# Kernel optimization log

Measured on AMD Instinct MI355X. Metric: run time of the kernel, lower is better.

Reference implementation:

```python
import jax, jax.numpy as jnp
import numpy as np

OFFSET_BINS = np.array([0.0, 0.00794435329, 0.0158887021, 0.0238330509, 0.0317773996,
                        0.0397217484, 0.0476660972, 0.0556104459, 0.0635547947,
                        0.0714991435, 0.08], dtype=np.float32)
BIN_WEIGHTS = jnp.array([0.16652107, 0.21488856, 0.37031708, 0.55618503, 0.75124664,
                         0.93943357, 1.07824539, 1.19423112, 1.55731375, 2.34173634],
                        dtype=jnp.float32)
RADIUS = 0.005
FAR = 1.0e5
EPS = 1e-7


def setup_inputs():
    key = jax.random.key(0)
    ks = jax.random.split(key, 10)
    B, N, M, C = 4, 2048, 4096, 5
    return {
        'pred_grasps': jax.random.normal(ks[0], (B, N, 4, 4), jnp.float32) * 0.1,
        'pred_scores': jax.random.uniform(ks[1], (B, N, 1), jnp.float32, 1e-4, 1.0 - 1e-4),
        'pred_points': jax.random.uniform(ks[2], (B, N, 3), jnp.float32) * 0.1,
        'grasp_width_head': jax.random.normal(ks[3], (B, 10, N), jnp.float32),
        'pos_contact_points': jax.random.uniform(ks[4], (B, M, 3), jnp.float32) * 0.1,
        'pos_contact_width': jax.random.uniform(ks[5], (B, M), jnp.float32) * 0.08,
        'pos_contact_rot': jax.random.normal(ks[6], (B, M, 3, 3), jnp.float32),
        'pos_contact_trans': jax.random.uniform(ks[7], (B, M, 3), jnp.float32) * 0.1,
        'gripper_control_points': jax.random.normal(ks[8], (1, C, 3), jnp.float32) * 0.05,
        'gripper_control_points_sym': jax.random.normal(ks[9], (1, C, 3), jnp.float32) * 0.05,
        'epoch': 0,
    }


def _gather(a, idx):
    # a: (B, M, ...), idx: (B, N) -> (B, N, ...)
    return jax.vmap(lambda x, j: x[j])(a, idx)


def _pairwise_sq(a, b):
    # a: (B,N,3), b: (B,M,3) -> (B,N,M) squared distances via norm expansion
    an = jnp.sum(a * a, -1)
    bn = jnp.sum(b * b, -1)
    cross = jnp.einsum('bnd,bmd->bnm', a, b)
    return jnp.maximum(an[:, :, None] + bn[:, None, :] - 2.0 * cross, 0.0)


def _pair_min_cp(P, G):
    # P,G: (B,N,C,3) control point sets -> (B,N) min_j sum_{c,d}(P_i - G_j)^2
    pn = jnp.sum(P * P, axis=(2, 3))
    gn = jnp.sum(G * G, axis=(2, 3))
    cross = jnp.einsum('bicd,bjcd->bij', P, G)  # (B,N,N)
    sq = pn[:, :, None] + gn[:, None, :] - 2.0 * cross
    return jnp.min(sq, axis=2)


def _forward(pred_grasps, pred_scores, pred_points, grasp_width_head,
             pos_contact_points, pos_contact_width, pos_contact_rot,
             pos_contact_trans, gripper_control_points, gripper_control_points_sym):
    B, N, _ = pred_points.shape
    # ---- labels: nearest GT contact per predicted point (nsample=1) ----
    d2 = _pairwise_sq(pred_points, pos_contact_points)          # (B,N,M)
    idx = jnp.argmin(d2, axis=2)                                 # (B,N)
    min_d2 = jnp.take_along_axis(d2, idx[:, :, None], axis=2)[..., 0]
    width_label = _gather(pos_contact_width, idx)[..., None]     # (B,N,1)
    success = (min_d2 < RADIUS ** 2).astype(jnp.float32)[..., None]  # (B,N,1)
    rot_label = _gather(pos_contact_rot, idx)                    # (B,N,3,3)
    trans_label = _gather(pos_contact_trans, idx)                # (B,N,3)

    pos_in_view = jnp.clip(jnp.sum(success, axis=1), 1.0, None)  # (B,1)

    # ---- binary score loss with balanced pos/neg sampling ----
    p = jnp.clip(pred_scores, EPS, 1.0 - EPS)
    bce = -(success * jnp.log(p) + (1.0 - success) * jnp.log(1.0 - p))[..., 0]  # (B,N)
    pos = success[..., 0]
    neg = 1.0 - pos
    n_pos = jnp.sum(pos, axis=1)                                 # (B,)
    r = jax.random.uniform(jax.random.key(42), (B, N))
    pri = jnp.where(neg > 0.5, r, jnp.inf)
    rank = jnp.argsort(jnp.argsort(pri, axis=1), axis=1)         # random ranks over negatives
    k = jnp.where(n_pos > 0, n_pos, 2.0)
    sel_neg = ((rank < k[:, None]) & (neg > 0.5)).astype(jnp.float32)
    sel = pos + sel_neg
    bin_ce_loss = jnp.mean(jnp.sum(bce * sel, axis=1) / jnp.maximum(jnp.sum(sel, axis=1), 1.0))

    # ---- width loss: multihot bins + weighted BCE-with-logits ----
    lo = jnp.asarray(OFFSET_BINS[:-1])
    hi = jnp.asarray(OFFSET_BINS[1:])
    multihot = ((width_label >= lo) & (width_label < hi)).astype(jnp.float32)  # (B,N,10)
    x = jnp.transpose(grasp_width_head, (0, 2, 1))               # (B,N,10)
    bcew = jnp.maximum(x, 0.0) - x * multihot + jnp.log1p(jnp.exp(-jnp.abs(x)))
    wl = jnp.mean(BIN_WEIGHTS[None, None, :] * bcew, axis=2)     # (B,N)
    width_loss = jnp.mean(jnp.sum(wl * pos, axis=1, keepdims=True) / pos_in_view)

    # ---- ADD-S loss ----
    mask = success > 0.5                                          # (B,N,1)
    rot_l = jnp.where(mask[..., None], rot_label, FAR)
    trans_l = jnp.where(mask, trans_label, FAR)
    cp = gripper_control_points[0]                                # (C,3)
    cps = gripper_control_points_sym[0]
    pred_rot = pred_grasps[:, :, :3, :3]
    pred_trans = pred_grasps[:, :, :3, 3]
    P = jnp.einsum('bnij,cj->bnci', pred_rot, cp) + pred_trans[:, :, None, :]
    G = jnp.einsum('bnij,cj->bnci', rot_l, cp) + trans_l[:, :, None, :]
    Gs = jnp.einsum('bnij,cj->bnci', rot_l, cps) + trans_l[:, :, None, :]
    m = jnp.minimum(_pair_min_cp(P, G), _pair_min_cp(P, Gs))     # (B,N)
    min_adds = pos * jnp.sqrt(jnp.maximum(m, 0.0) + 1e-12)
    adds = jnp.sum(pred_scores[..., 0] * min_adds, axis=1) / pos_in_view[:, 0]
    adds_loss = jnp.mean(adds)

    total_loss = bin_ce_loss + width_loss + 3.0 * adds_loss
    return total_loss, bin_ce_loss, width_loss, adds_loss


def reference(pred_grasps, pred_scores, pred_points, grasp_width_head,
              pos_contact_points, pos_contact_width, pos_contact_rot,
              pos_contact_trans, gripper_control_points, gripper_control_points_sym, epoch):
    return _forward(pred_grasps, pred_scores, pred_points, grasp_width_head,
                    pos_contact_points, pos_contact_width, pos_contact_rot,
                    pos_contact_trans, gripper_control_points, gripper_control_points_sym)
```

## Files before the change

### kernel.cpp

```cpp
#include <hip/hip_runtime.h>
#include <math.h>

#define B_ 4
#define N_ 2048
#define M_ 4096

__constant__ float c_LO[10] = {0.0f, 0.00794435329f, 0.0158887021f, 0.0238330509f,
                               0.0317773996f, 0.0397217484f, 0.0476660972f,
                               0.0556104459f, 0.0635547947f, 0.0714991435f};
__constant__ float c_HI[10] = {0.00794435329f, 0.0158887021f, 0.0238330509f,
                               0.0317773996f, 0.0397217484f, 0.0476660972f,
                               0.0556104459f, 0.0635547947f, 0.0714991435f, 0.08f};
__constant__ float c_BW[10] = {0.16652107f, 0.21488856f, 0.37031708f, 0.55618503f,
                               0.75124664f, 0.93943357f, 1.07824539f, 1.19423112f,
                               1.55731375f, 2.34173634f};

#define R2_ 2.5e-05f
#define FAR_ 100000.0f
#define EPS_ 1e-07f

__device__ inline unsigned rotl32(unsigned x, int d) { return (x << d) | (x >> (32 - d)); }

__device__ inline void threefry2x32_42(unsigned x0, unsigned x1, unsigned& o0, unsigned& o1) {
    const unsigned k0 = 0u, k1 = 42u;
    const unsigned k2 = k0 ^ k1 ^ 0x1BD11BDAu;
    const unsigned ks[3] = {k0, k1, k2};
    const int rot[2][4] = {{13, 15, 26, 6}, {17, 29, 16, 24}};
    unsigned v0 = x0 + k0;
    unsigned v1 = x1 + k1;
#pragma unroll
    for (int i = 0; i < 5; ++i) {
        const int* r = rot[i & 1];
#pragma unroll
        for (int j = 0; j < 4; ++j) {
            v0 += v1;
            v1 = rotl32(v1, r[j]);
            v1 ^= v0;
        }
        v0 += ks[(i + 1) % 3];
        v1 += ks[(i + 2) % 3] + (unsigned)(i + 1);
    }
    o0 = v0; o1 = v1;
}

__device__ inline float bits_to_uniform(unsigned bits) {
    float f = __uint_as_float((bits >> 9) | 0x3f800000u) - 1.0f;
    return fmaxf(0.0f, f);
}

__device__ inline float jax_uniform_r(int flat) {
    unsigned o0, o1;
    if (flat < 4096) {
        threefry2x32_42((unsigned)flat, (unsigned)(flat + 4096), o0, o1);
        return bits_to_uniform(o0);
    } else {
        threefry2x32_42((unsigned)(flat - 4096), (unsigned)flat, o0, o1);
        return bits_to_uniform(o1);
    }
}

__global__ __launch_bounds__(256, 4) void nn_prep_kernel(
        const float* __restrict__ ppts, const float* __restrict__ pcp,
        const float* __restrict__ pred_grasps,
        const float* __restrict__ rot, const float* __restrict__ trans,
        const float* __restrict__ cp, const float* __restrict__ cps,
        int* __restrict__ idx_out, float* __restrict__ d2_out,
        float* __restrict__ Pout, float* __restrict__ Gout) {
    int blk = blockIdx.x;
    int b = blk / (N_ / 8);
    int tile = blk % (N_ / 8);
    int tid = threadIdx.x;
    int ig = tid & 1;
    int part = tid >> 1;
    int i0 = tile * 8 + ig * 4;

    float ax[4], ay[4], az[4], an[4];
#pragma unroll
    for (int ii = 0; ii < 4; ++ii) {
        const float* pp = ppts + ((size_t)b * N_ + i0 + ii) * 3;
        ax[ii] = pp[0]; ay[ii] = pp[1]; az[ii] = pp[2];
        an[ii] = ax[ii] * ax[ii] + ay[ii] * ay[ii] + az[ii] * az[ii];
    }

    const float4* pb4 = reinterpret_cast<const float4*>(pcp + (size_t)b * M_ * 3);
    float best[4] = {INFINITY, INFINITY, INFINITY, INFINITY};
    int bidx[4] = {0, 0, 0, 0};
    for (int g = 0; g < 8; ++g) {
        int grp = g * 128 + part;
        float4 q0 = pb4[grp * 3 + 0];
        float4 q1 = pb4[grp * 3 + 1];
        float4 q2 = pb4[grp * 3 + 2];
        float px[4] = {q0.x, q0.w, q1.z, q2.y};
        float py[4] = {q0.y, q1.x, q1.w, q2.z};
        float pz[4] = {q0.z, q1.y, q2.x, q2.w};
#pragma unroll
        for (int k = 0; k < 4; ++k) {
            float bn = px[k] * px[k] + py[k] * py[k] + pz[k] * pz[k];
            int j = grp * 4 + k;
#pragma unroll
            for (int ii = 0; ii < 4; ++ii) {
                float cross = ax[ii] * px[k] + ay[ii] * py[k] + az[ii] * pz[k];
                float d = an[ii] + bn - 2.0f * cross;
                d = fmaxf(d, 0.0f);
                if (d < best[ii]) { best[ii] = d; bidx[ii] = j; }
            }
        }
    }

    __shared__ float sd[8][128];
    __shared__ int si[8][128];
#pragma unroll
    for (int ii = 0; ii < 4; ++ii) {
        sd[ig * 4 + ii][part] = best[ii];
        si[ig * 4 + ii][part] = bidx[ii];
    }
    __syncthreads();

    if (tid < 8) {
        int n = tile * 8 + tid;
        float bb = INFINITY;
        int bi = 0x7fffffff;
        for (int p = 0; p < 128; ++p) {
            float dv = sd[tid][p];
            int iv = si[tid][p];
            if (dv < bb || (dv == bb && iv < bi)) { bb = dv; bi = iv; }
        }
        idx_out[b * N_ + n] = bi;
        d2_out[b * N_ + n] = bb;

        size_t i = (size_t)b * N_ + n;
        const float* g = pred_grasps + i * 16;
        float R[3][3] = {{g[0], g[1], g[2]}, {g[4], g[5], g[6]}, {g[8], g[9], g[10]}};
        float t[3] = {g[3], g[7], g[11]};

        float* P = Pout + i * 16;
        float pn = 0.0f;
#pragma unroll
        for (int c = 0; c < 5; ++c) {
            float cx = cp[c * 3], cy = cp[c * 3 + 1], cz = cp[c * 3 + 2];
#pragma unroll
            for (int kk = 0; kk < 3; ++kk) {
                float v = R[kk][0] * cx + R[kk][1] * cy + R[kk][2] * cz + t[kk];
                P[c * 3 + kk] = v;
                pn += v * v;
            }
        }
        P[15] = pn;

        bool succ = bb < R2_;
        float RL[3][3], TL[3];
        if (succ) {
            const float* rl = rot + ((size_t)b * M_ + bi) * 9;
#pragma unroll
            for (int a = 0; a < 3; ++a)
#pragma unroll
                for (int c2 = 0; c2 < 3; ++c2) RL[a][c2] = rl[a * 3 + c2];
            const float* tl = trans + ((size_t)b * M_ + bi) * 3;
            TL[0] = tl[0]; TL[1] = tl[1]; TL[2] = tl[2];
        } else {
#pragma unroll
            for (int a = 0; a < 3; ++a) {
#pragma unroll
                for (int c2 = 0; c2 < 3; ++c2) RL[a][c2] = FAR_;
                TL[a] = FAR_;
            }
        }

        float* G = Gout + i * 32;
        float gn = 0.0f, gsn = 0.0f;
#pragma unroll
        for (int c = 0; c < 5; ++c) {
            float cx = cp[c * 3], cy = cp[c * 3 + 1], cz = cp[c * 3 + 2];
#pragma unroll
            for (int kk = 0; kk < 3; ++kk) {
                float v = RL[kk][0] * cx + RL[kk][1] * cy + RL[kk][2] * cz + TL[kk];
                G[c * 3 + kk] = v;
                gn += v * v;
            }
        }
        G[15] = gn;
#pragma unroll
        for (int c = 0; c < 5; ++c) {
            float cx = cps[c * 3], cy = cps[c * 3 + 1], cz = cps[c * 3 + 2];
#pragma unroll
            for (int kk = 0; kk < 3; ++kk) {
                float v = RL[kk][0] * cx + RL[kk][1] * cy + RL[kk][2] * cz + TL[kk];
                G[16 + c * 3 + kk] = v;
                gsn += v * v;
            }
        }
        G[31] = gsn;
    }
}

__global__ __launch_bounds__(256) void rank_kernel(const float* __restrict__ d2w,
                                                   float* __restrict__ selws,
                                                   int* __restrict__ done_cnt) {
    if (blockIdx.x == 0 && threadIdx.x == 0) *done_cnt = 0;
    int blk = blockIdx.x;
    int b = blk / (N_ / 16);
    int tile = blk % (N_ / 16);
    int tid = threadIdx.x;
    int n_local = tid & 15;
    int part = tid >> 4;

    __shared__ __align__(16) float pri[N_];
    __shared__ int cnt_sh[16][17];
    __shared__ int s_npos;
    if (tid == 0) s_npos = 0;
    __syncthreads();

    int lp = 0;
    for (int q = tid; q < N_; q += 256) {
        bool pos = d2w[b * N_ + q] < R2_;
        pri[q] = pos ? INFINITY : jax_uniform_r(b * N_ + q);
        if (pos) lp++;
    }
    atomicAdd(&s_npos, lp);
    __syncthreads();

    int n = tile * 16 + n_local;
    float ra = pri[n];

    int cnt = 0;
    const float4* p4 = reinterpret_cast<const float4*>(pri);
    for (int o = 0; o < 8; ++o) {
        float4 v[4];
#pragma unroll
        for (int k = 0; k < 4; ++k) v[k] = p4[part + (o * 4 + k) * 16];
#pragma unroll
        for (int k = 0; k < 4; ++k) {
            int qb = (part + (o * 4 + k) * 16) * 4;
            cnt += ((v[k].x < ra) || (v[k].x == ra && (qb + 0) < n)) ? 1 : 0;
            cnt += ((v[k].y < ra) || (v[k].y == ra && (qb + 1) < n)) ? 1 : 0;
            cnt += ((v[k].z < ra) || (v[k].z == ra && (qb + 2) < n)) ? 1 : 0;
            cnt += ((v[k].w < ra) || (v[k].w == ra && (qb + 3) < n)) ? 1 : 0;
        }
    }
    cnt_sh[part][n_local] = cnt;
    __syncthreads();

    if (tid < 16) {
        int tot = 0;
#pragma unroll
        for (int p = 0; p < 16; ++p) tot += cnt_sh[p][tid];
        int npos = s_npos;
        int kk = (npos > 0) ? npos : 2;
        int n2 = tile * 16 + tid;
        float r2 = pri[n2];
        selws[b * N_ + n2] = (r2 == INFINITY) ? 1.0f : ((tot < kk) ? 1.0f : 0.0f);
    }
}

__global__ __launch_bounds__(256, 4) void adds_kernel(const float* __restrict__ Parr,
                                                      const float* __restrict__ Garr,
                                                      float* __restrict__ mOut) {
    int blk = blockIdx.x;
    int b = blk / (N_ / 8);
    int tile = blk % (N_ / 8);
    int ig = threadIdx.x & 1;
    int part = threadIdx.x >> 1;
    int i0 = tile * 8 + ig * 4;

    const float4* P4 = reinterpret_cast<const float4*>(Parr) + ((size_t)b * N_ + i0) * 4;
    float Pv[4][16];
#pragma unroll
    for (int ii = 0; ii < 4; ++ii) {
#pragma unroll
        for (int q = 0; q < 4; ++q) {
            float4 t4 = P4[ii * 4 + q];
            Pv[ii][q * 4 + 0] = t4.x; Pv[ii][q * 4 + 1] = t4.y;
            Pv[ii][q * 4 + 2] = t4.z; Pv[ii][q * 4 + 3] = t4.w;
        }
    }

    const float4* Gb4 = reinterpret_cast<const float4*>(Garr) + (size_t)b * N_ * 8;
    float best[4] = {INFINITY, INFINITY, INFINITY, INFINITY};
    int j0 = part * 16;
    for (int j = j0; j < j0 + 16; ++j) {
        const float4* G4 = Gb4 + (size_t)j * 8;
        float gg[16];
#pragma unroll
        for (int q = 0; q < 4; ++q) {
            float4 t4 = G4[q];
            gg[q * 4 + 0] = t4.x; gg[q * 4 + 1] = t4.y;
            gg[q * 4 + 2] = t4.z; gg[q * 4 + 3] = t4.w;
        }
        {
            float d[4] = {0.0f, 0.0f, 0.0f, 0.0f};
#pragma unroll
            for (int q = 0; q < 15; ++q)
#pragma unroll
                for (int ii = 0; ii < 4; ++ii) d[ii] += Pv[ii][q] * gg[q];
#pragma unroll
            for (int ii = 0; ii < 4; ++ii) {
                float s = Pv[ii][15] + gg[15] - 2.0f * d[ii];
                best[ii] = fminf(best[ii], s);
            }
        }
#pragma unroll
        for (int q = 0; q < 4; ++q) {
            float4 t4 = G4[4 + q];
            gg[q * 4 + 0] = t4.x; gg[q * 4 + 1] = t4.y;
            gg[q * 4 + 2] = t4.z; gg[q * 4 + 3] = t4.w;
        }
        {
            float d[4] = {0.0f, 0.0f, 0.0f, 0.0f};
#pragma unroll
            for (int q = 0; q < 15; ++q)
#pragma unroll
                for (int ii = 0; ii < 4; ++ii) d[ii] += Pv[ii][q] * gg[q];
#pragma unroll
            for (int ii = 0; ii < 4; ++ii) {
                float s = Pv[ii][15] + gg[15] - 2.0f * d[ii];
                best[ii] = fminf(best[ii], s);
            }
        }
    }
    __shared__ float sm[128][9];
#pragma unroll
    for (int ii = 0; ii < 4; ++ii) sm[part][ig * 4 + ii] = best[ii];
    __syncthreads();
    if (threadIdx.x < 8) {
        float bb = sm[0][threadIdx.x];
#pragma unroll
        for (int q = 1; q < 128; ++q) bb = fminf(bb, sm[q][threadIdx.x]);
        mOut[b * N_ + tile * 8 + threadIdx.x] = bb;
    }
}

__global__ __launch_bounds__(256) void finalize_kernel(
        const float* __restrict__ scores, const float* __restrict__ gwh,
        const float* __restrict__ pcw, const int* __restrict__ idxw,
        const float* __restrict__ d2w, const float* __restrict__ mw,
        const float* __restrict__ selws,
        float* __restrict__ partials, int* __restrict__ done_cnt,
        float* __restrict__ out) {
    int blk = blockIdx.x;
    int b = blk >> 3;
    int part = blk & 7;
    int tid = threadIdx.x;
    int n = part * 256 + tid;
    __shared__ float wsum[4][5];

    float sc = scores[b * N_ + n];
    float pcl = fminf(fmaxf(sc, EPS_), 0.9999999f);
    bool pos = d2w[b * N_ + n] < R2_;
    float s = pos ? 1.0f : 0.0f;
    float bce = -(s * logf(pcl) + (1.0f - s) * logf(1.0f - pcl));
    float selv = selws[b * N_ + n];
    float sum_sel = selv;
    float sum_bce = bce * selv;
    float sum_pos = s;
    float sum_wl = 0.0f, sum_adds = 0.0f;
    if (pos) {
        int jx = idxw[b * N_ + n];
        float w = pcw[b * M_ + jx];
        float acc = 0.0f;
#pragma unroll
        for (int jb = 0; jb < 10; ++jb) {
            float x = gwh[((size_t)b * 10 + jb) * N_ + n];
            float mh = (w >= c_LO[jb] && w < c_HI[jb]) ? 1.0f : 0.0f;
            float bw = fmaxf(x, 0.0f) - x * mh + log1pf(expf(-fabsf(x)));
            acc += c_BW[jb] * bw;
        }
        sum_wl = acc * 0.1f;
        float mv = mw[b * N_ + n];
        sum_adds = sc * sqrtf(fmaxf(mv, 0.0f) + 1e-12f);
    }

    float v0 = sum_sel, v1 = sum_bce, v2 = sum_wl, v3 = sum_adds, v4 = sum_pos;
#pragma unroll
    for (int off = 32; off > 0; off >>= 1) {
        v0 += __shfl_down(v0, off);
        v1 += __shfl_down(v1, off);
        v2 += __shfl_down(v2, off);
        v3 += __shfl_down(v3, off);
        v4 += __shfl_down(v4, off);
    }
    int wv = tid >> 6, lane = tid & 63;
    if (lane == 0) {
        wsum[wv][0] = v0; wsum[wv][1] = v1; wsum[wv][2] = v2; wsum[wv][3] = v3; wsum[wv][4] = v4;
    }
    __syncthreads();
    if (tid == 0) {
        float t0 = 0, t1 = 0, t2 = 0, t3 = 0, t4 = 0;
#pragma unroll
        for (int w = 0; w < 4; ++w) {
            t0 += wsum[w][0]; t1 += wsum[w][1]; t2 += wsum[w][2]; t3 += wsum[w][3]; t4 += wsum[w][4];
        }
        float* pp = partials + (size_t)blk * 5;
        pp[0] = t0; pp[1] = t1; pp[2] = t2; pp[3] = t3; pp[4] = t4;
        __threadfence();
        int old = atomicAdd(done_cnt, 1);
        if (old == B_ * 8 - 1) {
            __threadfence();
            float bin = 0, wid = 0, ad = 0;
#pragma unroll
            for (int b2 = 0; b2 < B_; ++b2) {
                float u0 = 0, u1 = 0, u2 = 0, u3 = 0, u4 = 0;
#pragma unroll
                for (int p2 = 0; p2 < 8; ++p2) {
                    const float* q = partials + (size_t)(b2 * 8 + p2) * 5;
                    u0 += q[0]; u1 += q[1]; u2 += q[2]; u3 += q[3]; u4 += q[4];
                }
                float piv = fmaxf(u4, 1.0f);
                bin += u1 / fmaxf(u0, 1.0f);
                wid += u2 / piv;
                ad  += u3 / piv;
            }
            bin *= 0.25f; wid *= 0.25f; ad *= 0.25f;
            out[0] = bin + wid + 3.0f * ad;
            out[1] = bin;
            out[2] = wid;
            out[3] = ad;
        }
    }
}

extern "C" void kernel_launch(void* const* d_in, const int* in_sizes, int n_in,
                              void* d_out, int out_size, void* d_ws, size_t ws_size,
                              hipStream_t stream) {
    const float* pred_grasps = (const float*)d_in[0];
    const float* pred_scores = (const float*)d_in[1];
    const float* pred_points = (const float*)d_in[2];
    const float* gwh         = (const float*)d_in[3];
    const float* pcp         = (const float*)d_in[4];
    const float* pcw         = (const float*)d_in[5];
    const float* pcr         = (const float*)d_in[6];
    const float* pct         = (const float*)d_in[7];
    const float* cp          = (const float*)d_in[8];
    const float* cps         = (const float*)d_in[9];
    (void)in_sizes; (void)n_in; (void)out_size; (void)ws_size;

    float* ws = (float*)d_ws;
    int*   idxw  = (int*)ws;
    float* d2w   = ws + 8192;
    float* Pw    = ws + 16384;
    float* Gw    = Pw + 131072;
    float* mw    = Gw + 262144;
    float* selws = mw + 8192;
    float* parts = selws + 8192;
    int*   done  = (int*)(parts + 160);
    float* outp  = (float*)d_out;

    hipLaunchKernelGGL(nn_prep_kernel, dim3(B_ * (N_ / 8)), dim3(256), 0, stream,
                       pred_points, pcp, pred_grasps, pcr, pct, cp, cps,
                       idxw, d2w, Pw, Gw);
    hipLaunchKernelGGL(rank_kernel, dim3(B_ * (N_ / 16)), dim3(256), 0, stream,
                       d2w, selws, done);
    hipLaunchKernelGGL(adds_kernel, dim3(B_ * (N_ / 8)), dim3(256), 0, stream,
                       Pw, Gw, mw);
    hipLaunchKernelGGL(finalize_kernel, dim3(B_ * 8), dim3(256), 0, stream,
                       pred_scores, gwh, pcw, idxw, d2w, mw, selws, parts, done, outp);
}
```

Baseline: 162.8 us.

## Fuse rank, adds and finalize kernels into one launch with counter-gated finalize

Merges the rank, ADD-S min-distance and finalize kernels into one mega kernel that dispatches on block index. Finalize blocks spin on a global counter until all producer blocks finish. The ADD-S part now stages G tiles in shared memory and gives each thread 2 P rows instead of 4, so all threads reuse the staged G. This removes two kernel launches and lets the rank and adds work run concurrently, at the cost of a spin-wait that depends on the finalize blocks being dispatched last and extra syncthreads per tile.

```diff
diff --git a/kernel.cpp b/kernel.cpp
--- a/kernel.cpp
+++ b/kernel.cpp
@@ -4,6 +4,11 @@
 #define B_ 4
 #define N_ 2048
 #define M_ 4096
+
+#define ADDS_BLOCKS (B_ * (N_ / 8))
+#define RANK_BLOCKS (B_ * (N_ / 16))
+#define FIN_BLOCKS (B_ * 8)
+#define PROD_BLOCKS (ADDS_BLOCKS + RANK_BLOCKS)
 
 __constant__ float c_LO[10] = {0.0f, 0.00794435329f, 0.0158887021f, 0.0238330509f,
                                0.0317773996f, 0.0397217484f, 0.0476660972f,
@@ -65,7 +70,9 @@
         const float* __restrict__ rot, const float* __restrict__ trans,
         const float* __restrict__ cp, const float* __restrict__ cps,
         int* __restrict__ idx_out, float* __restrict__ d2_out,
-        float* __restrict__ Pout, float* __restrict__ Gout) {
+        float* __restrict__ Pout, float* __restrict__ Gout,
+        int* __restrict__ counters) {
+    if (blockIdx.x == 0 && threadIdx.x == 0) { counters[0] = 0; counters[1] = 0; }
     int blk = blockIdx.x;
     int b = blk / (N_ / 8);
     int tile = blk % (N_ / 8);
@@ -193,227 +200,257 @@
     }
 }
 
-__global__ __launch_bounds__(256) void rank_kernel(const float* __restrict__ d2w,
-                                                   float* __restrict__ selws,
-                                                   int* __restrict__ done_cnt) {
-    if (blockIdx.x == 0 && threadIdx.x == 0) *done_cnt = 0;
-    int blk = blockIdx.x;
-    int b = blk / (N_ / 16);
-    int tile = blk % (N_ / 16);
-    int tid = threadIdx.x;
-    int n_local = tid & 15;
-    int part = tid >> 4;
-
-    __shared__ __align__(16) float pri[N_];
-    __shared__ int cnt_sh[16][17];
-    __shared__ int s_npos;
-    if (tid == 0) s_npos = 0;
-    __syncthreads();
-
-    int lp = 0;
-    for (int q = tid; q < N_; q += 256) {
-        bool pos = d2w[b * N_ + q] < R2_;
-        pri[q] = pos ? INFINITY : jax_uniform_r(b * N_ + q);
-        if (pos) lp++;
-    }
-    atomicAdd(&s_npos, lp);
-    __syncthreads();
-
-    int n = tile * 16 + n_local;
-    float ra = pri[n];
-
-    int cnt = 0;
-    const float4* p4 = reinterpret_cast<const float4*>(pri);
-    for (int o = 0; o < 8; ++o) {
-        float4 v[4];
-#pragma unroll
-        for (int k = 0; k < 4; ++k) v[k] = p4[part + (o * 4 + k) * 16];
-#pragma unroll
-        for (int k = 0; k < 4; ++k) {
-            int qb = (part + (o * 4 + k) * 16) * 4;
-            cnt += ((v[k].x < ra) || (v[k].x == ra && (qb + 0) < n)) ? 1 : 0;
-            cnt += ((v[k].y < ra) || (v[k].y == ra && (qb + 1) < n)) ? 1 : 0;
-            cnt += ((v[k].z < ra) || (v[k].z == ra && (qb + 2) < n)) ? 1 : 0;
-            cnt += ((v[k].w < ra) || (v[k].w == ra && (qb + 3) < n)) ? 1 : 0;
-        }
-    }
-    cnt_sh[part][n_local] = cnt;
-    __syncthreads();
-
-    if (tid < 16) {
-        int tot = 0;
-#pragma unroll
-        for (int p = 0; p < 16; ++p) tot += cnt_sh[p][tid];
-        int npos = s_npos;
-        int kk = (npos > 0) ? npos : 2;
-        int n2 = tile * 16 + tid;
-        float r2 = pri[n2];
-        selws[b * N_ + n2] = (r2 == INFINITY) ? 1.0f : ((tot < kk) ? 1.0f : 0.0f);
-    }
-}
-
-__global__ __launch_bounds__(256, 4) void adds_kernel(const float* __restrict__ Parr,
-                                                      const float* __restrict__ Garr,
-                                                      float* __restrict__ mOut) {
-    int blk = blockIdx.x;
-    int b = blk / (N_ / 8);
-    int tile = blk % (N_ / 8);
-    int ig = threadIdx.x & 1;
-    int part = threadIdx.x >> 1;
-    int i0 = tile * 8 + ig * 4;
-
-    const float4* P4 = reinterpret_cast<const float4*>(Parr) + ((size_t)b * N_ + i0) * 4;
-    float Pv[4][16];
-#pragma unroll
-    for (int ii = 0; ii < 4; ++ii) {
-#pragma unroll
-        for (int q = 0; q < 4; ++q) {
-            float4 t4 = P4[ii * 4 + q];
-            Pv[ii][q * 4 + 0] = t4.x; Pv[ii][q * 4 + 1] = t4.y;
-            Pv[ii][q * 4 + 2] = t4.z; Pv[ii][q * 4 + 3] = t4.w;
-        }
-    }
-
-    const float4* Gb4 = reinterpret_cast<const float4*>(Garr) + (size_t)b * N_ * 8;
-    float best[4] = {INFINITY, INFINITY, INFINITY, INFINITY};
-    int j0 = part * 16;
-    for (int j = j0; j < j0 + 16; ++j) {
-        const float4* G4 = Gb4 + (size_t)j * 8;
-        float gg[16];
-#pragma unroll
-        for (int q = 0; q < 4; ++q) {
-            float4 t4 = G4[q];
-            gg[q * 4 + 0] = t4.x; gg[q * 4 + 1] = t4.y;
-            gg[q * 4 + 2] = t4.z; gg[q * 4 + 3] = t4.w;
-        }
-        {
-            float d[4] = {0.0f, 0.0f, 0.0f, 0.0f};
-#pragma unroll
-            for (int q = 0; q < 15; ++q)
-#pragma unroll
-                for (int ii = 0; ii < 4; ++ii) d[ii] += Pv[ii][q] * gg[q];
-#pragma unroll
-            for (int ii = 0; ii < 4; ++ii) {
-                float s = Pv[ii][15] + gg[15] - 2.0f * d[ii];
-                best[ii] = fminf(best[ii], s);
-            }
-        }
-#pragma unroll
-        for (int q = 0; q < 4; ++q) {
-            float4 t4 = G4[4 + q];
-            gg[q * 4 + 0] = t4.x; gg[q * 4 + 1] = t4.y;
-            gg[q * 4 + 2] = t4.z; gg[q * 4 + 3] = t4.w;
-        }
-        {
-            float d[4] = {0.0f, 0.0f, 0.0f, 0.0f};
-#pragma unroll
-            for (int q = 0; q < 15; ++q)
-#pragma unroll
-                for (int ii = 0; ii < 4; ++ii) d[ii] += Pv[ii][q] * gg[q];
-#pragma unroll
-            for (int ii = 0; ii < 4; ++ii) {
-                float s = Pv[ii][15] + gg[15] - 2.0f * d[ii];
-                best[ii] = fminf(best[ii], s);
-            }
-        }
-    }
-    __shared__ float sm[128][9];
-#pragma unroll
-    for (int ii = 0; ii < 4; ++ii) sm[part][ig * 4 + ii] = best[ii];
-    __syncthreads();
-    if (threadIdx.x < 8) {
-        float bb = sm[0][threadIdx.x];
-#pragma unroll
-        for (int q = 1; q < 128; ++q) bb = fminf(bb, sm[q][threadIdx.x]);
-        mOut[b * N_ + tile * 8 + threadIdx.x] = bb;
-    }
-}
-
-__global__ __launch_bounds__(256) void finalize_kernel(
+__global__ __launch_bounds__(256, 4) void mega_kernel(
+        const float* __restrict__ Parr, const float* __restrict__ Garr,
+        float* __restrict__ mOut,
+        const float* __restrict__ d2w, float* __restrict__ selws,
         const float* __restrict__ scores, const float* __restrict__ gwh,
         const float* __restrict__ pcw, const int* __restrict__ idxw,
-        const float* __restrict__ d2w, const float* __restrict__ mw,
-        const float* __restrict__ selws,
-        float* __restrict__ partials, int* __restrict__ done_cnt,
+        float* __restrict__ partials, int* __restrict__ counters,
         float* __restrict__ out) {
-    int blk = blockIdx.x;
-    int b = blk >> 3;
-    int part = blk & 7;
+    __shared__ __align__(16) char smem[18464];
+    int bid = blockIdx.x;
     int tid = threadIdx.x;
-    int n = part * 256 + tid;
-    __shared__ float wsum[4][5];
-
-    float sc = scores[b * N_ + n];
-    float pcl = fminf(fmaxf(sc, EPS_), 0.9999999f);
-    bool pos = d2w[b * N_ + n] < R2_;
-    float s = pos ? 1.0f : 0.0f;
-    float bce = -(s * logf(pcl) + (1.0f - s) * logf(1.0f - pcl));
-    float selv = selws[b * N_ + n];
-    float sum_sel = selv;
-    float sum_bce = bce * selv;
-    float sum_pos = s;
-    float sum_wl = 0.0f, sum_adds = 0.0f;
-    if (pos) {
-        int jx = idxw[b * N_ + n];
-        float w = pcw[b * M_ + jx];
-        float acc = 0.0f;
-#pragma unroll
-        for (int jb = 0; jb < 10; ++jb) {
-            float x = gwh[((size_t)b * 10 + jb) * N_ + n];
-            float mh = (w >= c_LO[jb] && w < c_HI[jb]) ? 1.0f : 0.0f;
-            float bw = fmaxf(x, 0.0f) - x * mh + log1pf(expf(-fabsf(x)));
-            acc += c_BW[jb] * bw;
-        }
-        sum_wl = acc * 0.1f;
-        float mv = mw[b * N_ + n];
-        sum_adds = sc * sqrtf(fmaxf(mv, 0.0f) + 1e-12f);
-    }
-
-    float v0 = sum_sel, v1 = sum_bce, v2 = sum_wl, v3 = sum_adds, v4 = sum_pos;
-#pragma unroll
-    for (int off = 32; off > 0; off >>= 1) {
-        v0 += __shfl_down(v0, off);
-        v1 += __shfl_down(v1, off);
-        v2 += __shfl_down(v2, off);
-        v3 += __shfl_down(v3, off);
-        v4 += __shfl_down(v4, off);
-    }
-    int wv = tid >> 6, lane = tid & 63;
-    if (lane == 0) {
-        wsum[wv][0] = v0; wsum[wv][1] = v1; wsum[wv][2] = v2; wsum[wv][3] = v3; wsum[wv][4] = v4;
-    }
-    __syncthreads();
-    if (tid == 0) {
-        float t0 = 0, t1 = 0, t2 = 0, t3 = 0, t4 = 0;
-#pragma unroll
-        for (int w = 0; w < 4; ++w) {
-            t0 += wsum[w][0]; t1 += wsum[w][1]; t2 += wsum[w][2]; t3 += wsum[w][3]; t4 += wsum[w][4];
-        }
-        float* pp = partials + (size_t)blk * 5;
-        pp[0] = t0; pp[1] = t1; pp[2] = t2; pp[3] = t3; pp[4] = t4;
+
+    if (bid < ADDS_BLOCKS) {
+        int b = bid >> 8;
+        int tile_i = bid & 255;
+        int i0 = tile_i * 8;
+        int ip = tid & 3;
+        int jp = tid >> 2;
+
+        const float4* P4 = reinterpret_cast<const float4*>(Parr) +
+                           ((size_t)b * N_ + i0 + ip * 2) * 4;
+        float Pv[2][16];
+#pragma unroll
+        for (int h = 0; h < 2; ++h)
+#pragma unroll
+            for (int q = 0; q < 4; ++q) {
+                float4 v = P4[h * 4 + q];
+                Pv[h][q * 4 + 0] = v.x; Pv[h][q * 4 + 1] = v.y;
+                Pv[h][q * 4 + 2] = v.z; Pv[h][q * 4 + 3] = v.w;
+            }
+
+        float* sG = (float*)smem;
+        const float4* Gb4 = reinterpret_cast<const float4*>(Garr) + (size_t)b * N_ * 8;
+        float best[2] = {INFINITY, INFINITY};
+
+        for (int jt = 0; jt < 16; ++jt) {
+            __syncthreads();
+            const float4* src = Gb4 + (size_t)jt * 1024;
+#pragma unroll
+            for (int t = 0; t < 4; ++t) {
+                int idx = t * 256 + tid;
+                int r = idx >> 3, q = idx & 7;
+                float4 v = src[idx];
+                *reinterpret_cast<float4*>(&sG[r * 36 + q * 4]) = v;
+            }
+            __syncthreads();
+#pragma unroll
+            for (int jj = 0; jj < 2; ++jj) {
+                const float* row = &sG[(jj * 64 + jp) * 36];
+                float gg[16];
+#pragma unroll
+                for (int q = 0; q < 4; ++q) {
+                    float4 v = *reinterpret_cast<const float4*>(&row[q * 4]);
+                    gg[q * 4 + 0] = v.x; gg[q * 4 + 1] = v.y;
+                    gg[q * 4 + 2] = v.z; gg[q * 4 + 3] = v.w;
+                }
+                {
+                    float d0 = 0.0f, d1 = 0.0f;
+#pragma unroll
+                    for (int q = 0; q < 15; ++q) {
+                        d0 += Pv[0][q] * gg[q];
+                        d1 += Pv[1][q] * gg[q];
+                    }
+                    best[0] = fminf(best[0], Pv[0][15] + gg[15] - 2.0f * d0);
+                    best[1] = fminf(best[1], Pv[1][15] + gg[15] - 2.0f * d1);
+                }
+#pragma unroll
+                for (int q = 0; q < 4; ++q) {
+                    float4 v = *reinterpret_cast<const float4*>(&row[16 + q * 4]);
+                    gg[q * 4 + 0] = v.x; gg[q * 4 + 1] = v.y;
+                    gg[q * 4 + 2] = v.z; gg[q * 4 + 3] = v.w;
+                }
+                {
+                    float d0 = 0.0f, d1 = 0.0f;
+#pragma unroll
+                    for (int q = 0; q < 15; ++q) {
+                        d0 += Pv[0][q] * gg[q];
+                        d1 += Pv[1][q] * gg[q];
+                    }
+                    best[0] = fminf(best[0], Pv[0][15] + gg[15] - 2.0f * d0);
+                    best[1] = fminf(best[1], Pv[1][15] + gg[15] - 2.0f * d1);
+                }
+            }
+        }
+
+        __syncthreads();
+        float* sm = (float*)smem;
+        sm[jp * 9 + ip * 2 + 0] = best[0];
+        sm[jp * 9 + ip * 2 + 1] = best[1];
+        __syncthreads();
+        if (tid < 8) {
+            float bb = sm[tid];
+            for (int q = 1; q < 64; ++q) bb = fminf(bb, sm[q * 9 + tid]);
+            mOut[b * N_ + i0 + tid] = bb;
+        }
+        __syncthreads();
+        if (tid == 0) {
+            __threadfence();
+            __hip_atomic_fetch_add(&counters[0], 1, __ATOMIC_RELEASE,
+                                   __HIP_MEMORY_SCOPE_AGENT);
+        }
+    } else if (bid < PROD_BLOCKS) {
+        int rid = bid - ADDS_BLOCKS;
+        int b = rid / (N_ / 16);
+        int tile = rid % (N_ / 16);
+        int n_local = tid & 15;
+        int part = tid >> 4;
+
+        float* pri = (float*)smem;
+        int* cnt_sh = (int*)(smem + 8192);
+        __shared__ int s_npos;
+        if (tid == 0) s_npos = 0;
+        __syncthreads();
+
+        int lp = 0;
+        for (int q = tid; q < N_; q += 256) {
+            bool pos = d2w[b * N_ + q] < R2_;
+            pri[q] = pos ? INFINITY : jax_uniform_r(b * N_ + q);
+            if (pos) lp++;
+        }
+        atomicAdd(&s_npos, lp);
+        __syncthreads();
+
+        int n = tile * 16 + n_local;
+        float ra = pri[n];
+
+        int cnt = 0;
+        const float4* p4 = reinterpret_cast<const float4*>(pri);
+        for (int o = 0; o < 8; ++o) {
+            float4 v[4];
+#pragma unroll
+            for (int k = 0; k < 4; ++k) v[k] = p4[part + (o * 4 + k) * 16];
+#pragma unroll
+            for (int k = 0; k < 4; ++k) {
+                int qb = (part + (o * 4 + k) * 16) * 4;
+                cnt += ((v[k].x < ra) || (v[k].x == ra && (qb + 0) < n)) ? 1 : 0;
+                cnt += ((v[k].y < ra) || (v[k].y == ra && (qb + 1) < n)) ? 1 : 0;
+                cnt += ((v[k].z < ra) || (v[k].z == ra && (qb + 2) < n)) ? 1 : 0;
+                cnt += ((v[k].w < ra) || (v[k].w == ra && (qb + 3) < n)) ? 1 : 0;
+            }
+        }
+        cnt_sh[part * 17 + n_local] = cnt;
+        __syncthreads();
+
+        if (tid < 16) {
+            int tot = 0;
+#pragma unroll
+            for (int p = 0; p < 16; ++p) tot += cnt_sh[p * 17 + tid];
+            int npos = s_npos;
+            int kk = (npos > 0) ? npos : 2;
+            int n2 = tile * 16 + tid;
+            float r2 = pri[n2];
+            selws[b * N_ + n2] = (r2 == INFINITY) ? 1.0f : ((tot < kk) ? 1.0f : 0.0f);
+        }
+        __syncthreads();
+        if (tid == 0) {
+            __threadfence();
+            __hip_atomic_fetch_add(&counters[0], 1, __ATOMIC_RELEASE,
+                                   __HIP_MEMORY_SCOPE_AGENT);
+        }
+    } else {
+        int fid = bid - PROD_BLOCKS;
+        int b = fid >> 3;
+        int part = fid & 7;
+        int n = part * 256 + tid;
+        __shared__ float wsum[4][5];
+
+        if (tid == 0) {
+            while (__hip_atomic_load(&counters[0], __ATOMIC_ACQUIRE,
+                                     __HIP_MEMORY_SCOPE_AGENT) < PROD_BLOCKS) {
+                __builtin_amdgcn_s_sleep(2);
+            }
+        }
+        __syncthreads();
         __threadfence();
-        int old = atomicAdd(done_cnt, 1);
-        if (old == B_ * 8 - 1) {
+
+        float sc = scores[b * N_ + n];
+        float pcl = fminf(fmaxf(sc, EPS_), 0.9999999f);
+        bool pos = d2w[b * N_ + n] < R2_;
+        float s = pos ? 1.0f : 0.0f;
+        float bce = -(s * logf(pcl) + (1.0f - s) * logf(1.0f - pcl));
+        float selv = selws[b * N_ + n];
+        float sum_sel = selv;
+        float sum_bce = bce * selv;
+        float sum_pos = s;
+        float sum_wl = 0.0f, sum_adds = 0.0f;
+        if (pos) {
+            int jx = idxw[b * N_ + n];
+            float w = pcw[b * M_ + jx];
+            float acc = 0.0f;
+#pragma unroll
+            for (int jb = 0; jb < 10; ++jb) {
+                float x = gwh[((size_t)b * 10 + jb) * N_ + n];
+                float mh = (w >= c_LO[jb] && w < c_HI[jb]) ? 1.0f : 0.0f;
+                float bw = fmaxf(x, 0.0f) - x * mh + log1pf(expf(-fabsf(x)));
+                acc += c_BW[jb] * bw;
+            }
+            sum_wl = acc * 0.1f;
+            float mv = mOut[b * N_ + n];
+            sum_adds = sc * sqrtf(fmaxf(mv, 0.0f) + 1e-12f);
+        }
+
+        float v0 = sum_sel, v1 = sum_bce, v2 = sum_wl, v3 = sum_adds, v4 = sum_pos;
+#pragma unroll
+        for (int off = 32; off > 0; off >>= 1) {
+            v0 += __shfl_down(v0, off);
+            v1 += __shfl_down(v1, off);
+            v2 += __shfl_down(v2, off);
+            v3 += __shfl_down(v3, off);
+            v4 += __shfl_down(v4, off);
+        }
+        int wv = tid >> 6, lane = tid & 63;
+        if (lane == 0) {
+            wsum[wv][0] = v0; wsum[wv][1] = v1; wsum[wv][2] = v2;
+            wsum[wv][3] = v3; wsum[wv][4] = v4;
+        }
+        __syncthreads();
+        if (tid == 0) {
+            float t0 = 0, t1 = 0, t2 = 0, t3 = 0, t4 = 0;
+#pragma unroll
+            for (int w = 0; w < 4; ++w) {
+                t0 += wsum[w][0]; t1 += wsum[w][1]; t2 += wsum[w][2];
+                t3 += wsum[w][3]; t4 += wsum[w][4];
+            }
+            float* pp = partials + (size_t)fid * 5;
+            pp[0] = t0; pp[1] = t1; pp[2] = t2; pp[3] = t3; pp[4] = t4;
             __threadfence();
-            float bin = 0, wid = 0, ad = 0;
-#pragma unroll
-            for (int b2 = 0; b2 < B_; ++b2) {
-                float u0 = 0, u1 = 0, u2 = 0, u3 = 0, u4 = 0;
-#pragma unroll
-                for (int p2 = 0; p2 < 8; ++p2) {
-                    const float* q = partials + (size_t)(b2 * 8 + p2) * 5;
-                    u0 += q[0]; u1 += q[1]; u2 += q[2]; u3 += q[3]; u4 += q[4];
+            int old = __hip_atomic_fetch_add(&counters[1], 1, __ATOMIC_ACQ_REL,
+                                             __HIP_MEMORY_SCOPE_AGENT);
+            if (old == FIN_BLOCKS - 1) {
+                __threadfence();
+                float bin = 0, wid = 0, ad = 0;
+#pragma unroll
+                for (int b2 = 0; b2 < B_; ++b2) {
+                    float u0 = 0, u1 = 0, u2 = 0, u3 = 0, u4 = 0;
+#pragma unroll
+                    for (int p2 = 0; p2 < 8; ++p2) {
+                        const float* q = partials + (size_t)(b2 * 8 + p2) * 5;
+                        u0 += q[0]; u1 += q[1]; u2 += q[2]; u3 += q[3]; u4 += q[4];
+                    }
+                    float piv = fmaxf(u4, 1.0f);
+                    bin += u1 / fmaxf(u0, 1.0f);
+                    wid += u2 / piv;
+                    ad  += u3 / piv;
                 }
-                float piv = fmaxf(u4, 1.0f);
-                bin += u1 / fmaxf(u0, 1.0f);
-                wid += u2 / piv;
-                ad  += u3 / piv;
-            }
-            bin *= 0.25f; wid *= 0.25f; ad *= 0.25f;
-            out[0] = bin + wid + 3.0f * ad;
-            out[1] = bin;
-            out[2] = wid;
-            out[3] = ad;
+                bin *= 0.25f; wid *= 0.25f; ad *= 0.25f;
+                out[0] = bin + wid + 3.0f * ad;
+                out[1] = bin;
+                out[2] = wid;
+                out[3] = ad;
+            }
         }
     }
 }
@@ -441,16 +478,13 @@
     float* mw    = Gw + 262144;
     float* selws = mw + 8192;
     float* parts = selws + 8192;
-    int*   done  = (int*)(parts + 160);
+    int*   ctrs  = (int*)(parts + 160);
     float* outp  = (float*)d_out;
 
     hipLaunchKernelGGL(nn_prep_kernel, dim3(B_ * (N_ / 8)), dim3(256), 0, stream,
                        pred_points, pcp, pred_grasps, pcr, pct, cp, cps,
-                       idxw, d2w, Pw, Gw);
-    hipLaunchKernelGGL(rank_kernel, dim3(B_ * (N_ / 16)), dim3(256), 0, stream,
-                       d2w, selws, done);
-    hipLaunchKernelGGL(adds_kernel, dim3(B_ * (N_ / 8)), dim3(256), 0, stream,
-                       Pw, Gw, mw);
-    hipLaunchKernelGGL(finalize_kernel, dim3(B_ * 8), dim3(256), 0, stream,
-                       pred_scores, gwh, pcw, idxw, d2w, mw, selws, parts, done, outp);
-}
+                       idxw, d2w, Pw, Gw, ctrs);
+    hipLaunchKernelGGL(mega_kernel, dim3(PROD_BLOCKS + FIN_BLOCKS), dim3(256), 0, stream,
+                       Pw, Gw, mw, d2w, selws,
+                       pred_scores, gwh, pcw, idxw, parts, ctrs, outp);
+}
```

New measurement: 187.8 us. +15.4%, slower.

## Transpose G layout for coalesced adds loads and fold rank into finalize

Applied to the files above, without the earlier changes.

G control-point sets are now stored component-major (32 x N per batch), so the adds kernel can give each lane its own j and read coalesced loads. Each wave handles 2 predictions and reduces with wave shuffles instead of a shared-memory min. The separate rank kernel is removed and its selection counting moves into finalize, which saves one launch. The cost is that each finalize thread now does a serial 2048-element comparison loop across only 32 blocks, which may become the critical path.

```diff
diff --git a/kernel.cpp b/kernel.cpp
--- a/kernel.cpp
+++ b/kernel.cpp
@@ -65,7 +65,9 @@
         const float* __restrict__ rot, const float* __restrict__ trans,
         const float* __restrict__ cp, const float* __restrict__ cps,
         int* __restrict__ idx_out, float* __restrict__ d2_out,
-        float* __restrict__ Pout, float* __restrict__ Gout) {
+        float* __restrict__ Pout, float* __restrict__ Gt,
+        int* __restrict__ counters) {
+    if (blockIdx.x == 0 && threadIdx.x == 0) { counters[0] = 0; counters[1] = 0; }
     int blk = blockIdx.x;
     int b = blk / (N_ / 8);
     int tile = blk % (N_ / 8);
@@ -166,7 +168,7 @@
             }
         }
 
-        float* G = Gout + i * 32;
+        float* gtb = Gt + (size_t)b * 32 * N_ + n;
         float gn = 0.0f, gsn = 0.0f;
 #pragma unroll
         for (int c = 0; c < 5; ++c) {
@@ -174,158 +176,76 @@
 #pragma unroll
             for (int kk = 0; kk < 3; ++kk) {
                 float v = RL[kk][0] * cx + RL[kk][1] * cy + RL[kk][2] * cz + TL[kk];
-                G[c * 3 + kk] = v;
+                gtb[(size_t)(c * 3 + kk) * N_] = v;
                 gn += v * v;
             }
         }
-        G[15] = gn;
+        gtb[(size_t)15 * N_] = gn;
 #pragma unroll
         for (int c = 0; c < 5; ++c) {
             float cx = cps[c * 3], cy = cps[c * 3 + 1], cz = cps[c * 3 + 2];
 #pragma unroll
             for (int kk = 0; kk < 3; ++kk) {
                 float v = RL[kk][0] * cx + RL[kk][1] * cy + RL[kk][2] * cz + TL[kk];
-                G[16 + c * 3 + kk] = v;
+                gtb[(size_t)(16 + c * 3 + kk) * N_] = v;
                 gsn += v * v;
             }
         }
-        G[31] = gsn;
-    }
-}
-
-__global__ __launch_bounds__(256) void rank_kernel(const float* __restrict__ d2w,
-                                                   float* __restrict__ selws,
-                                                   int* __restrict__ done_cnt) {
-    if (blockIdx.x == 0 && threadIdx.x == 0) *done_cnt = 0;
-    int blk = blockIdx.x;
-    int b = blk / (N_ / 16);
-    int tile = blk % (N_ / 16);
-    int tid = threadIdx.x;
-    int n_local = tid & 15;
-    int part = tid >> 4;
-
-    __shared__ __align__(16) float pri[N_];
-    __shared__ int cnt_sh[16][17];
-    __shared__ int s_npos;
-    if (tid == 0) s_npos = 0;
-    __syncthreads();
-
-    int lp = 0;
-    for (int q = tid; q < N_; q += 256) {
-        bool pos = d2w[b * N_ + q] < R2_;
-        pri[q] = pos ? INFINITY : jax_uniform_r(b * N_ + q);
-        if (pos) lp++;
-    }
-    atomicAdd(&s_npos, lp);
-    __syncthreads();
-
-    int n = tile * 16 + n_local;
-    float ra = pri[n];
-
-    int cnt = 0;
-    const float4* p4 = reinterpret_cast<const float4*>(pri);
-    for (int o = 0; o < 8; ++o) {
-        float4 v[4];
-#pragma unroll
-        for (int k = 0; k < 4; ++k) v[k] = p4[part + (o * 4 + k) * 16];
-#pragma unroll
-        for (int k = 0; k < 4; ++k) {
-            int qb = (part + (o * 4 + k) * 16) * 4;
-            cnt += ((v[k].x < ra) || (v[k].x == ra && (qb + 0) < n)) ? 1 : 0;
-            cnt += ((v[k].y < ra) || (v[k].y == ra && (qb + 1) < n)) ? 1 : 0;
-            cnt += ((v[k].z < ra) || (v[k].z == ra && (qb + 2) < n)) ? 1 : 0;
-            cnt += ((v[k].w < ra) || (v[k].w == ra && (qb + 3) < n)) ? 1 : 0;
-        }
-    }
-    cnt_sh[part][n_local] = cnt;
-    __syncthreads();
-
-    if (tid < 16) {
-        int tot = 0;
-#pragma unroll
-        for (int p = 0; p < 16; ++p) tot += cnt_sh[p][tid];
-        int npos = s_npos;
-        int kk = (npos > 0) ? npos : 2;
-        int n2 = tile * 16 + tid;
-        float r2 = pri[n2];
-        selws[b * N_ + n2] = (r2 == INFINITY) ? 1.0f : ((tot < kk) ? 1.0f : 0.0f);
+        gtb[(size_t)31 * N_] = gsn;
     }
 }
 
 __global__ __launch_bounds__(256, 4) void adds_kernel(const float* __restrict__ Parr,
-                                                      const float* __restrict__ Garr,
+                                                      const float* __restrict__ Gt,
                                                       float* __restrict__ mOut) {
     int blk = blockIdx.x;
     int b = blk / (N_ / 8);
     int tile = blk % (N_ / 8);
-    int ig = threadIdx.x & 1;
-    int part = threadIdx.x >> 1;
-    int i0 = tile * 8 + ig * 4;
+    int w = threadIdx.x >> 6;
+    int lane = threadIdx.x & 63;
+    int i0 = tile * 8 + w * 2;
 
     const float4* P4 = reinterpret_cast<const float4*>(Parr) + ((size_t)b * N_ + i0) * 4;
-    float Pv[4][16];
-#pragma unroll
-    for (int ii = 0; ii < 4; ++ii) {
+    float Pv[2][16];
+#pragma unroll
+    for (int h = 0; h < 2; ++h)
 #pragma unroll
         for (int q = 0; q < 4; ++q) {
-            float4 t4 = P4[ii * 4 + q];
-            Pv[ii][q * 4 + 0] = t4.x; Pv[ii][q * 4 + 1] = t4.y;
-            Pv[ii][q * 4 + 2] = t4.z; Pv[ii][q * 4 + 3] = t4.w;
-        }
-    }
-
-    const float4* Gb4 = reinterpret_cast<const float4*>(Garr) + (size_t)b * N_ * 8;
-    float best[4] = {INFINITY, INFINITY, INFINITY, INFINITY};
-    int j0 = part * 16;
-    for (int j = j0; j < j0 + 16; ++j) {
-        const float4* G4 = Gb4 + (size_t)j * 8;
-        float gg[16];
-#pragma unroll
-        for (int q = 0; q < 4; ++q) {
-            float4 t4 = G4[q];
-            gg[q * 4 + 0] = t4.x; gg[q * 4 + 1] = t4.y;
-            gg[q * 4 + 2] = t4.z; gg[q * 4 + 3] = t4.w;
-        }
-        {
-            float d[4] = {0.0f, 0.0f, 0.0f, 0.0f};
-#pragma unroll
-            for (int q = 0; q < 15; ++q)
-#pragma unroll
-                for (int ii = 0; ii < 4; ++ii) d[ii] += Pv[ii][q] * gg[q];
-#pragma unroll
-            for (int ii = 0; ii < 4; ++ii) {
-                float s = Pv[ii][15] + gg[15] - 2.0f * d[ii];
-                best[ii] = fminf(best[ii], s);
-            }
-        }
-#pragma unroll
-        for (int q = 0; q < 4; ++q) {
-            float4 t4 = G4[4 + q];
-            gg[q * 4 + 0] = t4.x; gg[q * 4 + 1] = t4.y;
-            gg[q * 4 + 2] = t4.z; gg[q * 4 + 3] = t4.w;
-        }
-        {
-            float d[4] = {0.0f, 0.0f, 0.0f, 0.0f};
-#pragma unroll
-            for (int q = 0; q < 15; ++q)
-#pragma unroll
-                for (int ii = 0; ii < 4; ++ii) d[ii] += Pv[ii][q] * gg[q];
-#pragma unroll
-            for (int ii = 0; ii < 4; ++ii) {
-                float s = Pv[ii][15] + gg[15] - 2.0f * d[ii];
-                best[ii] = fminf(best[ii], s);
-            }
-        }
-    }
-    __shared__ float sm[128][9];
-#pragma unroll
-    for (int ii = 0; ii < 4; ++ii) sm[part][ig * 4 + ii] = best[ii];
-    __syncthreads();
-    if (threadIdx.x < 8) {
-        float bb = sm[0][threadIdx.x];
-#pragma unroll
-        for (int q = 1; q < 128; ++q) bb = fminf(bb, sm[q][threadIdx.x]);
-        mOut[b * N_ + tile * 8 + threadIdx.x] = bb;
+            float4 v = P4[h * 4 + q];
+            Pv[h][q * 4 + 0] = v.x; Pv[h][q * 4 + 1] = v.y;
+            Pv[h][q * 4 + 2] = v.z; Pv[h][q * 4 + 3] = v.w;
+        }
+
+    const float* gtb = Gt + (size_t)b * 32 * N_;
+    float best0 = INFINITY, best1 = INFINITY;
+    for (int jb = 0; jb < N_ / 64; ++jb) {
+        int j = jb * 64 + lane;
+        float g[32];
+#pragma unroll
+        for (int c = 0; c < 32; ++c) g[c] = gtb[(size_t)c * N_ + j];
+        float d00 = 0.0f, d01 = 0.0f, d10 = 0.0f, d11 = 0.0f;
+#pragma unroll
+        for (int q = 0; q < 15; ++q) {
+            d00 += Pv[0][q] * g[q];
+            d01 += Pv[0][q] * g[16 + q];
+            d10 += Pv[1][q] * g[q];
+            d11 += Pv[1][q] * g[16 + q];
+        }
+        float s00 = Pv[0][15] + g[15] - 2.0f * d00;
+        float s01 = Pv[0][15] + g[31] - 2.0f * d01;
+        float s10 = Pv[1][15] + g[15] - 2.0f * d10;
+        float s11 = Pv[1][15] + g[31] - 2.0f * d11;
+        best0 = fminf(best0, fminf(s00, s01));
+        best1 = fminf(best1, fminf(s10, s11));
+    }
+#pragma unroll
+    for (int m = 32; m > 0; m >>= 1) {
+        best0 = fminf(best0, __shfl_xor(best0, m));
+        best1 = fminf(best1, __shfl_xor(best1, m));
+    }
+    if (lane == 0) {
+        mOut[b * N_ + i0 + 0] = best0;
+        mOut[b * N_ + i0 + 1] = best1;
     }
 }
 
@@ -333,22 +253,55 @@
         const float* __restrict__ scores, const float* __restrict__ gwh,
         const float* __restrict__ pcw, const int* __restrict__ idxw,
         const float* __restrict__ d2w, const float* __restrict__ mw,
-        const float* __restrict__ selws,
-        float* __restrict__ partials, int* __restrict__ done_cnt,
+        float* __restrict__ partials, int* __restrict__ counters,
         float* __restrict__ out) {
-    int blk = blockIdx.x;
-    int b = blk >> 3;
-    int part = blk & 7;
+    int fid = blockIdx.x;
+    int b = fid >> 3;
+    int part = fid & 7;
     int tid = threadIdx.x;
     int n = part * 256 + tid;
+
+    __shared__ __align__(16) float pri[N_];
     __shared__ float wsum[4][5];
+    __shared__ int s_npos;
+    if (tid == 0) s_npos = 0;
+    __syncthreads();
+
+    int lp = 0;
+    for (int q = tid; q < N_; q += 256) {
+        bool posq = d2w[b * N_ + q] < R2_;
+        pri[q] = posq ? INFINITY : jax_uniform_r(b * N_ + q);
+        if (posq) lp++;
+    }
+    atomicAdd(&s_npos, lp);
+    __syncthreads();
+
+    float ra = pri[n];
+    int npos = s_npos;
+    int kk = (npos > 0) ? npos : 2;
+
+    float selv;
+    if (ra == INFINITY) {
+        selv = 1.0f;
+    } else {
+        int cnt = 0;
+        const float4* p4 = reinterpret_cast<const float4*>(pri);
+        for (int k4 = 0; k4 < N_ / 4; ++k4) {
+            float4 v = p4[k4];
+            int qb = k4 * 4;
+            cnt += ((v.x < ra) || (v.x == ra && (qb + 0) < n)) ? 1 : 0;
+            cnt += ((v.y < ra) || (v.y == ra && (qb + 1) < n)) ? 1 : 0;
+            cnt += ((v.z < ra) || (v.z == ra && (qb + 2) < n)) ? 1 : 0;
+            cnt += ((v.w < ra) || (v.w == ra && (qb + 3) < n)) ? 1 : 0;
+        }
+        selv = (cnt < kk) ? 1.0f : 0.0f;
+    }
 
     float sc = scores[b * N_ + n];
     float pcl = fminf(fmaxf(sc, EPS_), 0.9999999f);
     bool pos = d2w[b * N_ + n] < R2_;
     float s = pos ? 1.0f : 0.0f;
     float bce = -(s * logf(pcl) + (1.0f - s) * logf(1.0f - pcl));
-    float selv = selws[b * N_ + n];
     float sum_sel = selv;
     float sum_bce = bce * selv;
     float sum_pos = s;
@@ -380,20 +333,22 @@
     }
     int wv = tid >> 6, lane = tid & 63;
     if (lane == 0) {
-        wsum[wv][0] = v0; wsum[wv][1] = v1; wsum[wv][2] = v2; wsum[wv][3] = v3; wsum[wv][4] = v4;
+        wsum[wv][0] = v0; wsum[wv][1] = v1; wsum[wv][2] = v2;
+        wsum[wv][3] = v3; wsum[wv][4] = v4;
     }
     __syncthreads();
     if (tid == 0) {
         float t0 = 0, t1 = 0, t2 = 0, t3 = 0, t4 = 0;
 #pragma unroll
         for (int w = 0; w < 4; ++w) {
-            t0 += wsum[w][0]; t1 += wsum[w][1]; t2 += wsum[w][2]; t3 += wsum[w][3]; t4 += wsum[w][4];
-        }
-        float* pp = partials + (size_t)blk * 5;
+            t0 += wsum[w][0]; t1 += wsum[w][1]; t2 += wsum[w][2];
+            t3 += wsum[w][3]; t4 += wsum[w][4];
+        }
+        float* pp = partials + (size_t)fid * 5;
         pp[0] = t0; pp[1] = t1; pp[2] = t2; pp[3] = t3; pp[4] = t4;
         __threadfence();
-        int old = atomicAdd(done_cnt, 1);
-        if (old == B_ * 8 - 1) {
+        int old = atomicAdd(&counters[1], 1);
+        if (old == 32 - 1) {
             __threadfence();
             float bin = 0, wid = 0, ad = 0;
 #pragma unroll
@@ -437,20 +392,17 @@
     int*   idxw  = (int*)ws;
     float* d2w   = ws + 8192;
     float* Pw    = ws + 16384;
-    float* Gw    = Pw + 131072;
-    float* mw    = Gw + 262144;
-    float* selws = mw + 8192;
-    float* parts = selws + 8192;
-    int*   done  = (int*)(parts + 160);
+    float* Gt    = Pw + 131072;
+    float* mw    = Gt + 262144;
+    float* parts = mw + 8192;
+    int*   ctrs  = (int*)(parts + 160);
     float* outp  = (float*)d_out;
 
     hipLaunchKernelGGL(nn_prep_kernel, dim3(B_ * (N_ / 8)), dim3(256), 0, stream,
                        pred_points, pcp, pred_grasps, pcr, pct, cp, cps,
-                       idxw, d2w, Pw, Gw);
-    hipLaunchKernelGGL(rank_kernel, dim3(B_ * (N_ / 16)), dim3(256), 0, stream,
-                       d2w, selws, done);
+                       idxw, d2w, Pw, Gt, ctrs);
     hipLaunchKernelGGL(adds_kernel, dim3(B_ * (N_ / 8)), dim3(256), 0, stream,
-                       Pw, Gw, mw);
+                       Pw, Gt, mw);
     hipLaunchKernelGGL(finalize_kernel, dim3(B_ * 8), dim3(256), 0, stream,
-                       pred_scores, gwh, pcw, idxw, d2w, mw, selws, parts, done, outp);
-}
+                       pred_scores, gwh, pcw, idxw, d2w, mw, parts, ctrs, outp);
+}
```

After: 234.7 us. 1.44x slower.
